# Optimization experiments

Measured on AMD Instinct MI355X. Metric: run time of the kernel, lower is better.

Reference implementation:

```python
import jax, jax.numpy as jnp
import numpy as np

B = 16384      # batch of protein embeddings
C = 128        # n_channels
F = 5000       # number of GO terms (functions)
E_CHILD = 15000  # parent->child edges (~3 children per term)


def setup_inputs() -> dict:
    key = jax.random.key(0)
    k_x, k_w, k_p, k_c = jax.random.split(key, 4)
    x = jax.random.normal(k_x, (B, C), dtype=jnp.float32)
    W = jax.random.normal(k_w, (C, F), dtype=jnp.float32) * 0.05
    b = jnp.zeros((F,), dtype=jnp.float32)
    # random GO DAG edges; every node also gets a self-edge so the max
    # aggregation covers {self} U children, exactly like the torch loop
    parents = jax.random.randint(k_p, (E_CHILD,), 0, F, dtype=jnp.int32)
    childs = jax.random.randint(k_c, (E_CHILD,), 0, F, dtype=jnp.int32)
    self_idx = jnp.arange(F, dtype=jnp.int32)
    edge_parent = jnp.concatenate([self_idx, parents])  # [20000]
    edge_child = jnp.concatenate([self_idx, childs])    # [20000]
    return {"x": x, "W": W, "b": b,
            "edge_parent": edge_parent, "edge_child": edge_child}


def reference(x, W, b, edge_parent, edge_child):
    # Fused version of the 5000 separate Linear(C,1)+Sigmoid heads
    probs = jax.nn.sigmoid(x @ W + b)          # [B, F]
    # Hierarchical max over {self} U children via segment-max on edge list
    vals = probs.T[edge_child]                  # [E, B]
    agg = jax.ops.segment_max(vals, edge_parent, num_segments=F)  # [F, B]
    return agg.T                                # [B, F]
```

## Files before the change

### kernel.cpp

```cpp
#include <hip/hip_runtime.h>
#include <hip/hip_bf16.h>

#define BDIM 16384
#define CDIM 128
#define FDIM 5000
#define EDIM 20000
#define ELLW 16
#define MAXOVF 20000
#define NT4  10

typedef __attribute__((ext_vector_type(8))) short short8;
typedef __attribute__((ext_vector_type(4))) float f32x4;
typedef __attribute__((ext_vector_type(2))) float f32x2;
typedef __attribute__((ext_vector_type(2))) int i32x2;
typedef __attribute__((ext_vector_type(8))) unsigned short upk8;
typedef __attribute__((ext_vector_type(4))) unsigned short upk4;
typedef __attribute__((ext_vector_type(2))) unsigned int u32x2;

__device__ __forceinline__ unsigned short f2bf(float f) {
    unsigned int u = __builtin_bit_cast(unsigned int, f);
    u = (u + 0x7fffu + ((u >> 16) & 1u)) >> 16;
    return (unsigned short)u;
}
__device__ __forceinline__ float bf2f(unsigned short s) {
    unsigned int u = ((unsigned int)s) << 16;
    return __builtin_bit_cast(float, u);
}
__device__ __forceinline__ upk8 umax8(upk8 a, upk8 b) {
#if __has_builtin(__builtin_elementwise_max)
    return __builtin_elementwise_max(a, b);
#else
    upk8 r;
    #pragma unroll
    for (int j = 0; j < 8; ++j) r[j] = a[j] > b[j] ? a[j] : b[j];
    return r;
#endif
}
__device__ __forceinline__ upk4 umax4(upk4 a, upk4 b) {
#if __has_builtin(__builtin_elementwise_max)
    return __builtin_elementwise_max(a, b);
#else
    upk4 r;
    #pragma unroll
    for (int j = 0; j < 4; ++j) r[j] = a[j] > b[j] ? a[j] : b[j];
    return r;
#endif
}
__device__ __forceinline__ float fast_rcp(float x) {
#if __has_builtin(__builtin_amdgcn_rcpf)
    return __builtin_amdgcn_rcpf(x);
#else
    return 1.0f / x;
#endif
}
__device__ __forceinline__ unsigned int key2(unsigned int h) {
    unsigned int t = (h >> 15) & 0x00010001u;
    return h ^ (t * 0x7FFFu + 0x80008000u);
}
__device__ __forceinline__ unsigned short unkey(unsigned short k) {
    unsigned int s = (k >> 15) & 1u;
    return (unsigned short)(k ^ (0x8000u + ((s ^ 1u) * 0x7FFFu)));
}
__device__ __forceinline__ float sigk(unsigned short k) {
    return fast_rcp(1.0f + __expf(-bf2f(unkey(k))));
}
__device__ __forceinline__ void gll16(const unsigned short* g, unsigned short* l) {
    __builtin_amdgcn_global_load_lds(
        (const __attribute__((address_space(1))) void*)g,
        (__attribute__((address_space(3))) void*)l, 16, 0, 0);
}

__global__ __launch_bounds__(256) void prep1_kernel(
    const float* __restrict__ x, const float* __restrict__ W,
    unsigned short* __restrict__ xb, unsigned short* __restrict__ wt,
    unsigned short* __restrict__ ell, int* __restrict__ cur,
    int* __restrict__ ovf_cnt)
{
    __shared__ float lt[128][33];
    int bid = blockIdx.x, tid = threadIdx.x;
    if (bid < 1024) {
        size_t base = (size_t)bid * 2048 + (size_t)tid * 8;
        const f32x4* p = (const f32x4*)(x + base);
        f32x4 v0 = p[0], v1 = p[1];
        short8 o;
        o[0] = (short)f2bf(v0[0]); o[1] = (short)f2bf(v0[1]);
        o[2] = (short)f2bf(v0[2]); o[3] = (short)f2bf(v0[3]);
        o[4] = (short)f2bf(v1[0]); o[5] = (short)f2bf(v1[1]);
        o[6] = (short)f2bf(v1[2]); o[7] = (short)f2bf(v1[3]);
        *(short8*)(xb + base) = o;
    } else if (bid < 1181) {
        int f0 = (bid - 1024) * 32;
        int f_l = tid & 31, k0 = (tid >> 5) * 16;
        #pragma unroll
        for (int i = 0; i < 16; ++i) {
            int f = f0 + f_l;
            lt[k0 + i][f_l] = (f < FDIM) ? W[(size_t)(k0 + i) * FDIM + f] : 0.f;
        }
        __syncthreads();
        int f_l2 = tid >> 3, ks = (tid & 7) * 16;
        int f = f0 + f_l2;
        if (f < FDIM) {
            short8 o0, o1;
            #pragma unroll
            for (int j = 0; j < 8; ++j) o0[j] = (short)f2bf(lt[ks + j][f_l2]);
            #pragma unroll
            for (int j = 0; j < 8; ++j) o1[j] = (short)f2bf(lt[ks + 8 + j][f_l2]);
            *(short8*)(wt + (size_t)f * 128 + ks)     = o0;
            *(short8*)(wt + (size_t)f * 128 + ks + 8) = o1;
        }
    } else {
        int p = (bid - 1181) * 256 + tid;
        if (p < FDIM) {
            upk8 s;
            #pragma unroll
            for (int j = 0; j < 8; ++j) s[j] = (unsigned short)p;
            *(upk8*)(ell + (size_t)p * ELLW)     = s;
            *(upk8*)(ell + (size_t)p * ELLW + 8) = s;
            cur[p] = 1;
        }
        if (p == FDIM) *ovf_cnt = 0;
    }
}

__global__ __launch_bounds__(256) void prep2_kernel(
    const int* __restrict__ epar, const int* __restrict__ echild,
    int* __restrict__ cur, unsigned short* __restrict__ ell,
    int* __restrict__ ovf_cnt, int* __restrict__ ovf_pairs)
{
    int i = blockIdx.x * 256 + threadIdx.x;
    if (i < EDIM) {
        int p = epar[i], c = echild[i];
        if (p != c) {
            int pos = atomicAdd(&cur[p], 1);
            if (pos < ELLW) {
                ell[(size_t)p * ELLW + pos] = (unsigned short)c;
            } else {
                int j = atomicAdd(ovf_cnt, 1);
                if (j < MAXOVF) { ovf_pairs[2 * j] = p; ovf_pairs[2 * j + 1] = c; }
            }
        }
    }
}

__global__ __launch_bounds__(512, 4) void gemm8h_kernel(
    const unsigned short* __restrict__ xb,
    const unsigned short* __restrict__ wt,
    const float* __restrict__ bias,
    unsigned short* __restrict__ probs16)
{
    __shared__ unsigned short lA[128 * 128];
    __shared__ unsigned short lB[128 * 128];

    int bid0 = blockIdx.x;
    int bid  = (bid0 & 7) * (128 * NT4 / 8) + (bid0 >> 3);
    int bm = bid / NT4, bq = bid % NT4;
    int tid = threadIdx.x;
    int lane = tid & 63, w = tid >> 6;
    int wm = w >> 2, wn = w & 3;
    int g = lane >> 4, lr = lane & 15;
    int lrow = lane >> 4;
    int lcol = (lane & 15) << 4;

    auto stageA = [&]() {
        #pragma unroll
        for (int it = 0; it < 4; ++it) {
            int ci = w * 4 + it;
            int row = ci * 4 + lrow;
            int sw = lcol ^ ((row & 7) << 4);
            gll16(xb + ((size_t)(bm * 128 + row) << 7) + (sw >> 1),
                  lA + ci * 512);
        }
    };
    auto stageB = [&](int bn) {
        #pragma unroll
        for (int it = 0; it < 4; ++it) {
            int ci = w * 4 + it;
            int row = ci * 4 + lrow;
            int sw = lcol ^ ((row & 7) << 4);
            gll16(wt + ((size_t)(bn * 128 + row) << 7) + (sw >> 1),
                  lB + ci * 512);
        }
    };
    auto compute = [&](f32x4 (&acc)[4][2]) {
        #pragma unroll
        for (int ks = 0; ks < 4; ++ks) {
            int cbk = ks * 64 + g * 16;
            short8 af[4], bf[2];
            #pragma unroll
            for (int mi = 0; mi < 4; ++mi) {
                int row = wm * 64 + mi * 16 + lr;
                af[mi] = *(const short8*)((const char*)lA + row * 256 + (cbk ^ ((row & 7) << 4)));
            }
            #pragma unroll
            for (int nj = 0; nj < 2; ++nj) {
                int row = wn * 32 + nj * 16 + lr;
                bf[nj] = *(const short8*)((const char*)lB + row * 256 + (cbk ^ ((row & 7) << 4)));
            }
            #pragma unroll
            for (int mi = 0; mi < 4; ++mi)
                #pragma unroll
                for (int nj = 0; nj < 2; ++nj)
                    acc[mi][nj] = __builtin_amdgcn_mfma_f32_16x16x32_bf16(
                        af[mi], bf[nj], acc[mi][nj], 0, 0, 0);
        }
    };
    auto epilogue = [&](int bn, f32x4 (&acc)[4][2]) {
        #pragma unroll
        for (int nj = 0; nj < 2; ++nj) {
            int f = bn * 128 + wn * 32 + nj * 16 + lr;
            bool ok = (f < FDIM);
            float bb = ok ? bias[f] : 0.f;
            #pragma unroll
            for (int mi = 0; mi < 4; ++mi) {
                float z0 = acc[mi][nj][0] + bb;
                float z1 = acc[mi][nj][1] + bb;
                float z2 = acc[mi][nj][2] + bb;
                float z3 = acc[mi][nj][3] + bb;
                unsigned int h01, h23;
                asm("v_cvt_pk_bf16_f32 %0, %1, %2" : "=v"(h01) : "v"(z0), "v"(z1));
                asm("v_cvt_pk_bf16_f32 %0, %1, %2" : "=v"(h23) : "v"(z2), "v"(z3));
                u32x2 st;
                st[0] = key2(h01);
                st[1] = key2(h23);
                if (ok) {
                    int slab = bm * 16 + wm * 8 + mi * 2 + (g >> 1);
                    int grp  = slab * 2 + (g & 1);
                    *(u32x2*)(probs16 + ((size_t)grp * FDIM + f) * 4) = st;
                }
            }
        }
    };

    stageA();
    stageB(bq * 4);
    __syncthreads();

    f32x4 zero = {0.f, 0.f, 0.f, 0.f};
    for (int t = 0; t < 4; ++t) {
        f32x4 acc[4][2];
        #pragma unroll
        for (int mi = 0; mi < 4; ++mi) { acc[mi][0] = zero; acc[mi][1] = zero; }
        compute(acc);
        if (t < 3) {
            __syncthreads();
            stageB(bq * 4 + t + 1);
            epilogue(bq * 4 + t, acc);
            __syncthreads();
        } else {
            epilogue(bq * 4 + t, acc);
        }
    }
}

__global__ __launch_bounds__(1024) void segmax16_kernel(
    const unsigned short* __restrict__ probs16,
    const int* __restrict__ cur, const unsigned short* __restrict__ ell,
    const int* __restrict__ ovf_cnt, const int* __restrict__ ovf_pairs,
    float* __restrict__ out)
{
    __shared__ unsigned short l[FDIM * 4];
    int grp = blockIdx.x;
    int b0 = (grp >> 1) * 8 + (grp & 1) * 4;
    int tid = threadIdx.x;
    const unsigned short* src = probs16 + (size_t)grp * FDIM * 4;

    for (int c = tid; c < FDIM / 2; c += 1024) {
        gll16(src + (size_t)c * 8, l + (size_t)c * 8);
    }
    __syncthreads();

    int novf = *ovf_cnt; if (novf > MAXOVF) novf = MAXOVF;

    for (int p0 = tid * 2; p0 < FDIM; p0 += 2048) {
        int p1 = p0 + 1;
        i32x2 dg = *(const i32x2*)(cur + p0);
        upk4 ea = *(const upk4*)(ell + (size_t)p0 * ELLW);
        upk4 eb = *(const upk4*)(ell + (size_t)p1 * ELLW);
        upk4 ma = *(const upk4*)(l + (size_t)ea[0] * 4);
        upk4 mb = *(const upk4*)(l + (size_t)eb[0] * 4);
        ma = umax4(ma, *(const upk4*)(l + (size_t)ea[1] * 4));
        mb = umax4(mb, *(const upk4*)(l + (size_t)eb[1] * 4));
        ma = umax4(ma, *(const upk4*)(l + (size_t)ea[2] * 4));
        mb = umax4(mb, *(const upk4*)(l + (size_t)eb[2] * 4));
        ma = umax4(ma, *(const upk4*)(l + (size_t)ea[3] * 4));
        mb = umax4(mb, *(const upk4*)(l + (size_t)eb[3] * 4));
        if (dg[0] > 4) {
            upk4 e = *(const upk4*)(ell + (size_t)p0 * ELLW + 4);
            ma = umax4(ma, *(const upk4*)(l + (size_t)e[0] * 4));
            ma = umax4(ma, *(const upk4*)(l + (size_t)e[1] * 4));
            ma = umax4(ma, *(const upk4*)(l + (size_t)e[2] * 4));
            ma = umax4(ma, *(const upk4*)(l + (size_t)e[3] * 4));
        }
        if (dg[1] > 4) {
            upk4 e = *(const upk4*)(ell + (size_t)p1 * ELLW + 4);
            mb = umax4(mb, *(const upk4*)(l + (size_t)e[0] * 4));
            mb = umax4(mb, *(const upk4*)(l + (size_t)e[1] * 4));
            mb = umax4(mb, *(const upk4*)(l + (size_t)e[2] * 4));
            mb = umax4(mb, *(const upk4*)(l + (size_t)e[3] * 4));
        }
        if (dg[0] > 8) {
            upk8 e = *(const upk8*)(ell + (size_t)p0 * ELLW + 8);
            #pragma unroll
            for (int j = 0; j < 8; ++j)
                ma = umax4(ma, *(const upk4*)(l + (size_t)e[j] * 4));
        }
        if (dg[1] > 8) {
            upk8 e = *(const upk8*)(ell + (size_t)p1 * ELLW + 8);
            #pragma unroll
            for (int j = 0; j < 8; ++j)
                mb = umax4(mb, *(const upk4*)(l + (size_t)e[j] * 4));
        }
        if (dg[0] > ELLW) {
            for (int i = 0; i < novf; ++i)
                if (ovf_pairs[2 * i] == p0)
                    ma = umax4(ma, *(const upk4*)(l + (size_t)ovf_pairs[2 * i + 1] * 4));
        }
        if (dg[1] > ELLW) {
            for (int i = 0; i < novf; ++i)
                if (ovf_pairs[2 * i] == p1)
                    mb = umax4(mb, *(const upk4*)(l + (size_t)ovf_pairs[2 * i + 1] * 4));
        }
        size_t o = (size_t)b0 * FDIM + p0;
        #pragma unroll
        for (int r = 0; r < 4; ++r) {
            f32x2 v2;
            v2[0] = sigk(ma[r]);
            v2[1] = sigk(mb[r]);
            __builtin_nontemporal_store(v2, (f32x2*)(out + o + (size_t)r * FDIM));
        }
    }
}

extern "C" void kernel_launch(void* const* d_in, const int* in_sizes, int n_in,
                              void* d_out, int out_size, void* d_ws, size_t ws_size,
                              hipStream_t stream)
{
    const float* x     = (const float*)d_in[0];
    const float* W     = (const float*)d_in[1];
    const float* bias  = (const float*)d_in[2];
    const int*   epar  = (const int*)d_in[3];
    const int*   echild= (const int*)d_in[4];
    float* out = (float*)d_out;

    char* ws = (char*)d_ws;
    size_t off = 0;
    auto alloc = [&](size_t bytes) { size_t o = off; off = (off + bytes + 255) & ~(size_t)255; return o; };
    size_t o_probs  = alloc((size_t)BDIM * FDIM * 2);
    size_t o_xb     = alloc((size_t)BDIM * CDIM * 2);
    size_t o_wt     = alloc((size_t)FDIM * CDIM * 2);
    size_t o_ell    = alloc((size_t)FDIM * ELLW * 2);
    size_t o_cur    = alloc((size_t)FDIM * 4);
    size_t o_ovfc   = alloc(4);
    size_t o_ovfp   = alloc((size_t)MAXOVF * 8);
    (void)ws_size; (void)in_sizes; (void)n_in; (void)out_size;

    unsigned short* probs16 = (unsigned short*)(ws + o_probs);
    unsigned short* xb      = (unsigned short*)(ws + o_xb);
    unsigned short* wt      = (unsigned short*)(ws + o_wt);
    unsigned short* ell     = (unsigned short*)(ws + o_ell);
    int* cur      = (int*)(ws + o_cur);
    int* ovf_cnt  = (int*)(ws + o_ovfc);
    int* ovf_pairs= (int*)(ws + o_ovfp);

    prep1_kernel<<<1201, 256, 0, stream>>>(x, W, xb, wt, ell, cur, ovf_cnt);
    prep2_kernel<<<79, 256, 0, stream>>>(epar, echild, cur, ell, ovf_cnt, ovf_pairs);
    gemm8h_kernel<<<128 * NT4, 512, 0, stream>>>(xb, wt, bias, probs16);
    segmax16_kernel<<<BDIM / 8 * 2, 1024, 0, stream>>>(probs16, cur, ell,
                                                       ovf_cnt, ovf_pairs, out);
}
```

Before: 149.6 us.

## Sort parents by degree to cut divergence and exchange results through LDS

Adds a single-block prep kernel that counting-sorts parent nodes by child count and builds a permuted ELL table, so adjacent threads in segmax handle parents of similar degree and branch divergence drops. Segmax then writes per-parent maxima into a second LDS buffer indexed by original parent, syncs, and emits output with wider 16-byte stores in original order. The cost is an extra serial launch, 40KB more shared memory per block (possibly lowering occupancy), and an additional LDS round trip.

```diff
diff --git a/kernel.cpp b/kernel.cpp
--- a/kernel.cpp
+++ b/kernel.cpp
@@ -25,16 +25,6 @@
 __device__ __forceinline__ float bf2f(unsigned short s) {
     unsigned int u = ((unsigned int)s) << 16;
     return __builtin_bit_cast(float, u);
-}
-__device__ __forceinline__ upk8 umax8(upk8 a, upk8 b) {
-#if __has_builtin(__builtin_elementwise_max)
-    return __builtin_elementwise_max(a, b);
-#else
-    upk8 r;
-    #pragma unroll
-    for (int j = 0; j < 8; ++j) r[j] = a[j] > b[j] ? a[j] : b[j];
-    return r;
-#endif
 }
 __device__ __forceinline__ upk4 umax4(upk4 a, upk4 b) {
 #if __has_builtin(__builtin_elementwise_max)
@@ -139,6 +129,41 @@
                 if (j < MAXOVF) { ovf_pairs[2 * j] = p; ovf_pairs[2 * j + 1] = c; }
             }
         }
+    }
+}
+
+__global__ __launch_bounds__(1024) void prep3_kernel(
+    const int* __restrict__ cur, const unsigned short* __restrict__ ell,
+    unsigned int* __restrict__ dgp, unsigned short* __restrict__ ellp)
+{
+    __shared__ int hist[32];
+    __shared__ int base[32];
+    int tid = threadIdx.x;
+    if (tid < 32) hist[tid] = 0;
+    __syncthreads();
+    for (int p = tid; p < FDIM; p += 1024) {
+        int d = cur[p]; if (d > 31) d = 31;
+        atomicAdd(&hist[d], 1);
+    }
+    __syncthreads();
+    if (tid == 0) {
+        int acc = 0;
+        for (int b = 0; b < 32; ++b) { base[b] = acc; acc += hist[b]; }
+    }
+    __syncthreads();
+    for (int p = tid; p < FDIM; p += 1024) {
+        int d = cur[p]; if (d > 31) d = 31;
+        int pos = atomicAdd(&base[d], 1);
+        int dcap = cur[p]; if (dcap > 255) dcap = 255;
+        dgp[pos] = ((unsigned int)p << 8) | (unsigned int)dcap;
+    }
+    __syncthreads();
+    for (int i = tid; i < FDIM; i += 1024) {
+        int pr = (int)(dgp[i] >> 8);
+        upk8 lo = *(const upk8*)(ell + (size_t)pr * ELLW);
+        upk8 hi = *(const upk8*)(ell + (size_t)pr * ELLW + 8);
+        *(upk8*)(ellp + (size_t)i * ELLW)     = lo;
+        *(upk8*)(ellp + (size_t)i * ELLW + 8) = hi;
     }
 }
 
@@ -252,13 +277,15 @@
     }
 }
 
-__global__ __launch_bounds__(1024) void segmax16_kernel(
+__global__ __launch_bounds__(1024) void segmax17_kernel(
     const unsigned short* __restrict__ probs16,
-    const int* __restrict__ cur, const unsigned short* __restrict__ ell,
+    const unsigned int* __restrict__ dgp,
+    const unsigned short* __restrict__ ellp,
     const int* __restrict__ ovf_cnt, const int* __restrict__ ovf_pairs,
     float* __restrict__ out)
 {
     __shared__ unsigned short l[FDIM * 4];
+    __shared__ unsigned short xchg[FDIM * 4];
     int grp = blockIdx.x;
     int b0 = (grp >> 1) * 8 + (grp & 1) * 4;
     int tid = threadIdx.x;
@@ -271,11 +298,13 @@
 
     int novf = *ovf_cnt; if (novf > MAXOVF) novf = MAXOVF;
 
-    for (int p0 = tid * 2; p0 < FDIM; p0 += 2048) {
-        int p1 = p0 + 1;
-        i32x2 dg = *(const i32x2*)(cur + p0);
-        upk4 ea = *(const upk4*)(ell + (size_t)p0 * ELLW);
-        upk4 eb = *(const upk4*)(ell + (size_t)p1 * ELLW);
+    for (int w0 = tid * 2; w0 < FDIM; w0 += 2048) {
+        int w1 = w0 + 1;
+        u32x2 dv = *(const u32x2*)(dgp + w0);
+        int pa = (int)(dv[0] >> 8), da = (int)(dv[0] & 255u);
+        int pb = (int)(dv[1] >> 8), db = (int)(dv[1] & 255u);
+        upk8 ea = *(const upk8*)(ellp + (size_t)w0 * ELLW);
+        upk8 eb = *(const upk8*)(ellp + (size_t)w1 * ELLW);
         upk4 ma = *(const upk4*)(l + (size_t)ea[0] * 4);
         upk4 mb = *(const upk4*)(l + (size_t)eb[0] * 4);
         ma = umax4(ma, *(const upk4*)(l + (size_t)ea[1] * 4));
@@ -284,49 +313,59 @@
         mb = umax4(mb, *(const upk4*)(l + (size_t)eb[2] * 4));
         ma = umax4(ma, *(const upk4*)(l + (size_t)ea[3] * 4));
         mb = umax4(mb, *(const upk4*)(l + (size_t)eb[3] * 4));
-        if (dg[0] > 4) {
-            upk4 e = *(const upk4*)(ell + (size_t)p0 * ELLW + 4);
-            ma = umax4(ma, *(const upk4*)(l + (size_t)e[0] * 4));
-            ma = umax4(ma, *(const upk4*)(l + (size_t)e[1] * 4));
-            ma = umax4(ma, *(const upk4*)(l + (size_t)e[2] * 4));
-            ma = umax4(ma, *(const upk4*)(l + (size_t)e[3] * 4));
-        }
-        if (dg[1] > 4) {
-            upk4 e = *(const upk4*)(ell + (size_t)p1 * ELLW + 4);
-            mb = umax4(mb, *(const upk4*)(l + (size_t)e[0] * 4));
-            mb = umax4(mb, *(const upk4*)(l + (size_t)e[1] * 4));
-            mb = umax4(mb, *(const upk4*)(l + (size_t)e[2] * 4));
-            mb = umax4(mb, *(const upk4*)(l + (size_t)e[3] * 4));
-        }
-        if (dg[0] > 8) {
-            upk8 e = *(const upk8*)(ell + (size_t)p0 * ELLW + 8);
-            #pragma unroll
-            for (int j = 0; j < 8; ++j)
-                ma = umax4(ma, *(const upk4*)(l + (size_t)e[j] * 4));
-        }
-        if (dg[1] > 8) {
-            upk8 e = *(const upk8*)(ell + (size_t)p1 * ELLW + 8);
-            #pragma unroll
-            for (int j = 0; j < 8; ++j)
-                mb = umax4(mb, *(const upk4*)(l + (size_t)e[j] * 4));
-        }
-        if (dg[0] > ELLW) {
+        if (da > 4) {
+            ma = umax4(ma, *(const upk4*)(l + (size_t)ea[4] * 4));
+            ma = umax4(ma, *(const upk4*)(l + (size_t)ea[5] * 4));
+            ma = umax4(ma, *(const upk4*)(l + (size_t)ea[6] * 4));
+            ma = umax4(ma, *(const upk4*)(l + (size_t)ea[7] * 4));
+        }
+        if (db > 4) {
+            mb = umax4(mb, *(const upk4*)(l + (size_t)eb[4] * 4));
+            mb = umax4(mb, *(const upk4*)(l + (size_t)eb[5] * 4));
+            mb = umax4(mb, *(const upk4*)(l + (size_t)eb[6] * 4));
+            mb = umax4(mb, *(const upk4*)(l + (size_t)eb[7] * 4));
+        }
+        if (da > 8) {
+            upk8 e = *(const upk8*)(ellp + (size_t)w0 * ELLW + 8);
+            #pragma unroll
+            for (int k = 0; k < 8; ++k)
+                ma = umax4(ma, *(const upk4*)(l + (size_t)e[k] * 4));
+        }
+        if (db > 8) {
+            upk8 e = *(const upk8*)(ellp + (size_t)w1 * ELLW + 8);
+            #pragma unroll
+            for (int k = 0; k < 8; ++k)
+                mb = umax4(mb, *(const upk4*)(l + (size_t)e[k] * 4));
+        }
+        if (da > ELLW) {
             for (int i = 0; i < novf; ++i)
-                if (ovf_pairs[2 * i] == p0)
+                if (ovf_pairs[2 * i] == pa)
                     ma = umax4(ma, *(const upk4*)(l + (size_t)ovf_pairs[2 * i + 1] * 4));
         }
-        if (dg[1] > ELLW) {
+        if (db > ELLW) {
             for (int i = 0; i < novf; ++i)
-                if (ovf_pairs[2 * i] == p1)
+                if (ovf_pairs[2 * i] == pb)
                     mb = umax4(mb, *(const upk4*)(l + (size_t)ovf_pairs[2 * i + 1] * 4));
         }
+        *(upk4*)(xchg + (size_t)pa * 4) = ma;
+        *(upk4*)(xchg + (size_t)pb * 4) = mb;
+    }
+    __syncthreads();
+
+    for (int p0 = tid * 4; p0 < FDIM; p0 += 4096) {
+        upk4 m0 = *(const upk4*)(xchg + (size_t)p0 * 4);
+        upk4 m1 = *(const upk4*)(xchg + (size_t)(p0 + 1) * 4);
+        upk4 m2 = *(const upk4*)(xchg + (size_t)(p0 + 2) * 4);
+        upk4 m3 = *(const upk4*)(xchg + (size_t)(p0 + 3) * 4);
         size_t o = (size_t)b0 * FDIM + p0;
         #pragma unroll
         for (int r = 0; r < 4; ++r) {
-            f32x2 v2;
-            v2[0] = sigk(ma[r]);
-            v2[1] = sigk(mb[r]);
-            __builtin_nontemporal_store(v2, (f32x2*)(out + o + (size_t)r * FDIM));
+            f32x4 v4;
+            v4[0] = sigk(m0[r]);
+            v4[1] = sigk(m1[r]);
+            v4[2] = sigk(m2[r]);
+            v4[3] = sigk(m3[r]);
+            __builtin_nontemporal_store(v4, (f32x4*)(out + o + (size_t)r * FDIM));
         }
     }
 }
@@ -352,6 +391,8 @@
     size_t o_cur    = alloc((size_t)FDIM * 4);
     size_t o_ovfc   = alloc(4);
     size_t o_ovfp   = alloc((size_t)MAXOVF * 8);
+    size_t o_dgp    = alloc((size_t)FDIM * 4);
+    size_t o_ellp   = alloc((size_t)FDIM * ELLW * 2);
     (void)ws_size; (void)in_sizes; (void)n_in; (void)out_size;
 
     unsigned short* probs16 = (unsigned short*)(ws + o_probs);
@@ -361,10 +402,13 @@
     int* cur      = (int*)(ws + o_cur);
     int* ovf_cnt  = (int*)(ws + o_ovfc);
     int* ovf_pairs= (int*)(ws + o_ovfp);
+    unsigned int*   dgp  = (unsigned int*)(ws + o_dgp);
+    unsigned short* ellp = (unsigned short*)(ws + o_ellp);
 
     prep1_kernel<<<1201, 256, 0, stream>>>(x, W, xb, wt, ell, cur, ovf_cnt);
     prep2_kernel<<<79, 256, 0, stream>>>(epar, echild, cur, ell, ovf_cnt, ovf_pairs);
+    prep3_kernel<<<1, 1024, 0, stream>>>(cur, ell, dgp, ellp);
     gemm8h_kernel<<<128 * NT4, 512, 0, stream>>>(xb, wt, bias, probs16);
-    segmax16_kernel<<<BDIM / 8 * 2, 1024, 0, stream>>>(probs16, cur, ell,
+    segmax17_kernel<<<BDIM / 8 * 2, 1024, 0, stream>>>(probs16, dgp, ellp,
                                                        ovf_cnt, ovf_pairs, out);
 }
```

After: 148.2 us. No clear change (-1.0%).
